# Optimization experiments

Measured on AMD Instinct MI355X. Metric: run time of the kernel, lower is better.

Reference implementation:

```python
import jax, jax.numpy as jnp
import numpy as np

DIM = 2048
N_HEADS = 16
N_KV_HEADS = 4
HEAD_DIM = DIM // N_HEADS  # 128
N_REP = N_HEADS // N_KV_HEADS
LENS = [1024, 2048, 512, 512]
T = sum(LENS)  # 4096 packed tokens
THETA = 10000.0
NEG_INF = -1e30


def setup_inputs() -> dict:
    key = jax.random.key(0)
    ks = jax.random.split(key, 5)
    sd = 1.0 / np.sqrt(DIM)
    x = jax.random.normal(ks[0], (T, DIM), dtype=jnp.float32)
    wq = jax.random.normal(ks[1], (DIM, N_HEADS * HEAD_DIM), dtype=jnp.float32) * sd
    wk = jax.random.normal(ks[2], (DIM, N_KV_HEADS * HEAD_DIM), dtype=jnp.float32) * sd
    wv = jax.random.normal(ks[3], (DIM, N_KV_HEADS * HEAD_DIM), dtype=jnp.float32) * sd
    wo = jax.random.normal(ks[4], (N_HEADS * HEAD_DIM, DIM), dtype=jnp.float32) * sd
    # varlen packing metadata: per-token segment id and in-sequence position
    seq_ids = jnp.asarray(np.repeat(np.arange(len(LENS)), LENS), dtype=jnp.int32)
    pos = jnp.asarray(np.concatenate([np.arange(l) for l in LENS]), dtype=jnp.float32)
    # rotary frequencies (precompute_freqs_cis), gathered per packed token
    inv_freq = 1.0 / (THETA ** (np.arange(0, HEAD_DIM, 2, dtype=np.float32) / HEAD_DIM))  # [HEAD_DIM//2]
    angles = pos[:, None] * jnp.asarray(inv_freq)[None, :]  # [T, HEAD_DIM//2]
    freqs_cos = jnp.cos(angles)
    freqs_sin = jnp.sin(angles)
    return {"x": x, "wq": wq, "wk": wk, "wv": wv, "wo": wo,
            "freqs_cos": freqs_cos, "freqs_sin": freqs_sin, "seq_ids": seq_ids}


def _apply_rope(t, cos, sin):
    # t: [T, H, D]; rotate interleaved (even, odd) pairs, matching torch view_as_complex
    tr = t.reshape(t.shape[0], t.shape[1], HEAD_DIM // 2, 2)
    x0, x1 = tr[..., 0], tr[..., 1]
    c = cos[:, None, :]
    s = sin[:, None, :]
    o0 = x0 * c - x1 * s
    o1 = x0 * s + x1 * c
    return jnp.stack([o0, o1], axis=-1).reshape(t.shape)


def reference(x, wq, wk, wv, wo, freqs_cos, freqs_sin, seq_ids):
    Tn = x.shape[0]
    xq = (x @ wq).reshape(Tn, N_HEADS, HEAD_DIM)
    xk = (x @ wk).reshape(Tn, N_KV_HEADS, HEAD_DIM)
    xv = (x @ wv).reshape(Tn, N_KV_HEADS, HEAD_DIM)
    xq = _apply_rope(xq, freqs_cos, freqs_sin)
    xk = _apply_rope(xk, freqs_cos, freqs_sin)
    # GQA: repeat kv heads
    xk = jnp.repeat(xk, N_REP, axis=1)  # [T, N_HEADS, D]
    xv = jnp.repeat(xv, N_REP, axis=1)
    scale = 1.0 / jnp.sqrt(jnp.float32(HEAD_DIM))
    scores = jnp.einsum('thd,shd->hts', xq, xk) * scale  # [H, T, T]
    idx = jnp.arange(Tn)
    # varlen causal mask: same sequence AND key index <= query index
    allowed = (seq_ids[:, None] == seq_ids[None, :]) & (idx[None, :] <= idx[:, None])
    scores = jnp.where(allowed[None, :, :], scores, NEG_INF)
    attn = jax.nn.softmax(scores, axis=-1)
    out = jnp.einsum('hts,shd->thd', attn, xv).reshape(Tn, N_HEADS * HEAD_DIM)
    return out @ wo
```

## Files before the change

### kernel.cpp

```cpp
#include <hip/hip_runtime.h>
#include <hip/hip_bf16.h>


typedef __attribute__((ext_vector_type(4))) float f32x4;
typedef __attribute__((ext_vector_type(8))) short short8;
typedef __attribute__((ext_vector_type(4))) short short4v;

#define DEV __device__ __forceinline__

DEV short f2bf(float f) {
  __hip_bfloat16 h = __float2bfloat16(f);
  union { __hip_bfloat16 h; short s; } u; u.h = h; return u.s;
}
DEV float bf2f(short s) {
  union { short s; __hip_bfloat16 h; } u; u.s = s; return __bfloat162float(u.h);
}

DEV void gload_lds16(const void* g, void* l) {
  __builtin_amdgcn_global_load_lds(
      (const __attribute__((address_space(1))) void*)g,
      (__attribute__((address_space(3))) void*)l, 16, 0, 0);
}

__global__ void cast_x(const float* __restrict__ in, short* __restrict__ out, int n4) {
  int i = blockIdx.x * 256 + threadIdx.x;
  if (i >= n4) return;
  f32x4 v = ((const f32x4*)in)[i];
  short4v o;
  o[0] = f2bf(v[0]); o[1] = f2bf(v[1]); o[2] = f2bf(v[2]); o[3] = f2bf(v[3]);
  ((short4v*)out)[i] = o;
}

__global__ void transpose_cast_f32(const float* __restrict__ in, short* __restrict__ out,
                                   int R, int C) {
  __shared__ float tile[32][33];
  int bc = blockIdx.x * 32, br = blockIdx.y * 32;
  int tx = threadIdx.x, ty = threadIdx.y;
#pragma unroll
  for (int i = 0; i < 32; i += 8)
    tile[ty + i][tx] = in[(size_t)(br + ty + i) * C + bc + tx];
  __syncthreads();
#pragma unroll
  for (int i = 0; i < 32; i += 8)
    out[(size_t)(bc + ty + i) * R + br + tx] = f2bf(tile[tx][ty + i]);
}

__global__ void transpose_bf16(const short* __restrict__ in, short* __restrict__ out,
                               int R, int C, int ldi, int ldo) {
  __shared__ short tile[32][33];
  int bc = blockIdx.x * 32, br = blockIdx.y * 32;
  int tx = threadIdx.x, ty = threadIdx.y;
#pragma unroll
  for (int i = 0; i < 32; i += 8)
    tile[ty + i][tx] = in[(size_t)(br + ty + i) * ldi + bc + tx];
  __syncthreads();
#pragma unroll
  for (int i = 0; i < 32; i += 8)
    out[(size_t)(bc + ty + i) * ldo + br + tx] = tile[tx][ty + i];
}

__global__ void rope_kernel(short* __restrict__ qkv,
                            const float* __restrict__ fc, const float* __restrict__ fs) {
  int t = blockIdx.x;
  int g = threadIdx.x;
  int gi, col;
  if (g < 256) { int h = g >> 4; gi = g & 15; col = h * 128 + gi * 8; }
  else { int kh = (g - 256) >> 4; gi = (g - 256) & 15; col = 2048 + kh * 128 + gi * 8; }
  size_t base = (size_t)t * 3072 + col;
  short8 v = *(short8*)(qkv + base);
  f32x4 c = *(const f32x4*)(fc + (size_t)t * 64 + gi * 4);
  f32x4 s = *(const f32x4*)(fs + (size_t)t * 64 + gi * 4);
#pragma unroll
  for (int e = 0; e < 4; ++e) {
    float x0 = bf2f(v[2 * e]), x1 = bf2f(v[2 * e + 1]);
    float o0 = x0 * c[e] - x1 * s[e];
    float o1 = x0 * s[e] + x1 * c[e];
    v[2 * e] = f2bf(o0); v[2 * e + 1] = f2bf(o1);
  }
  *(short8*)(qkv + base) = v;
}

template <typename OutT>
__global__ __launch_bounds__(256, 2) void gemm_bt(const short* __restrict__ A,
                                                  const short* __restrict__ BT,
                                                  OutT* __restrict__ C,
                                                  int M, int N, int K,
                                                  int lda, int ldb, int ldc) {
  __shared__ short As[2][128 * 32];
  __shared__ short Bs[2][128 * 32];
  const int tid = threadIdx.x;
  const int wave = tid >> 6, lane = tid & 63;
  const int wr = wave >> 1, wc = wave & 1;
  const int bm = blockIdx.y, bn = blockIdx.x;
  const int l15 = lane & 15, l4 = lane >> 4;
  f32x4 acc[4][4] = {};

  auto stage = [&](int buf, int kt) {
#pragma unroll
    for (int i = 0; i < 2; ++i) {
      int j = wave * 2 + i;
      int row = j * 16 + (lane >> 2);
      int lg = (lane & 3) ^ ((row >> 1) & 3);
      gload_lds16(A + (size_t)(bm * 128 + row) * lda + kt + lg * 8, &As[buf][j * 512]);
      gload_lds16(BT + (size_t)(bn * 128 + row) * ldb + kt + lg * 8, &Bs[buf][j * 512]);
    }
  };

  stage(0, 0);
  __syncthreads();

  const int nk = K >> 5;
  for (int t = 0; t < nk; ++t) {
    const int cur = t & 1;
    if (t + 1 < nk) stage(cur ^ 1, (t + 1) * 32);

    short8 a[4], b[4];
#pragma unroll
    for (int m = 0; m < 4; ++m) {
      int row = wr * 64 + m * 16 + l15;
      int ph = l4 ^ ((row >> 1) & 3);
      a[m] = *(const short8*)(&As[cur][row * 32 + ph * 8]);
    }
#pragma unroll
    for (int n = 0; n < 4; ++n) {
      int row = wc * 64 + n * 16 + l15;
      int ph = l4 ^ ((row >> 1) & 3);
      b[n] = *(const short8*)(&Bs[cur][row * 32 + ph * 8]);
    }
    __builtin_amdgcn_s_setprio(1);
#pragma unroll
    for (int m = 0; m < 4; ++m)
#pragma unroll
      for (int n = 0; n < 4; ++n)
        acc[m][n] = __builtin_amdgcn_mfma_f32_16x16x32_bf16(a[m], b[n], acc[m][n], 0, 0, 0);
    __builtin_amdgcn_s_setprio(0);
    __syncthreads();
  }

#pragma unroll
  for (int m = 0; m < 4; ++m) {
    int row0 = bm * 128 + wr * 64 + m * 16 + l4 * 4;
#pragma unroll
    for (int n = 0; n < 4; ++n) {
      int col = bn * 128 + wc * 64 + n * 16 + l15;
#pragma unroll
      for (int r = 0; r < 4; ++r) {
        float v = acc[m][n][r];
        if constexpr (sizeof(OutT) == 4) C[(size_t)(row0 + r) * ldc + col] = v;
        else                             C[(size_t)(row0 + r) * ldc + col] = f2bf(v);
      }
    }
  }
}

__constant__ int QPERM[64] = {
    47, 46, 45, 44, 43, 42, 41, 40, 39, 38, 37, 36, 35, 34, 33, 32,
    31, 15, 30, 14, 29, 13, 28, 12, 27, 11, 26, 10, 25,  9, 24,  8,
    23,  7, 55, 63, 22,  6, 54, 62, 21,  5, 53, 61, 20,  4, 52, 60,
    19,  3, 51, 59, 18,  2, 50, 58, 17,  1, 49, 57, 16,  0, 48, 56};

__global__ __launch_bounds__(256, 3) void attn_kernel(const short* __restrict__ qkv,
                                                      const short* __restrict__ vt,
                                                      short* __restrict__ out) {
  __shared__ short Ks[64 * 128];
  __shared__ short Vs[128 * 64];
  __shared__ short Ps[4][16 * 64];
  const int tid = threadIdx.x;
  const int wave = tid >> 6, lane = tid & 63;
  const int l15 = lane & 15, l4 = lane >> 4;
  const int h = blockIdx.x;
  const int qi = QPERM[blockIdx.y];
  const int q0 = qi * 64;
  const int kvh = h >> 2;

  const int trow = q0 + wave * 16 + l15;
  short8 qf[4];
#pragma unroll
  for (int kk = 0; kk < 4; ++kk)
    qf[kk] = *(const short8*)(qkv + (size_t)trow * 3072 + h * 128 + kk * 32 + l4 * 8);

  f32x4 of[8] = {};
  float mrun[4], lrun[4];
#pragma unroll
  for (int r = 0; r < 4; ++r) { mrun[r] = -1e30f; lrun[r] = 0.f; }

  const int kstart = (q0 >= 3584) ? 3584 : (q0 >= 3072) ? 3072 : (q0 >= 1024) ? 1024 : 0;
  const int nt = ((q0 + 64) - kstart) >> 6;
  short* Pw = Ps[wave];

  const int krow0 = wave * 4 + (lane >> 4);
  const int ksl   = (lane & 15) ^ (krow0 & 7);
  const int vrow0 = wave * 8 + (lane >> 3);
  const int vsl   = (lane & 7) ^ (vrow0 & 7);

  short8 kreg[4], vreg[4];
  auto load_regs = [&](int kt) {
#pragma unroll
    for (int j = 0; j < 4; ++j) {
      kreg[j] = *(const short8*)(qkv + (size_t)(kt + j * 16 + krow0) * 3072 + 2048 +
                                 kvh * 128 + ksl * 8);
      vreg[j] = *(const short8*)(vt + (size_t)(kvh * 128 + j * 32 + vrow0) * 4096 + kt +
                                 vsl * 8);
    }
  };
  auto write_lds = [&]() {
#pragma unroll
    for (int j = 0; j < 4; ++j) {
      *(short8*)(Ks + (j * 16 + krow0) * 128 + (lane & 15) * 8) = kreg[j];
      *(short8*)(Vs + (j * 32 + vrow0) * 64 + (lane & 7) * 8) = vreg[j];
    }
  };

  load_regs(kstart);
  write_lds();
  __syncthreads();

  constexpr float SCL2 = 0.08838834764831845f * 1.4426950408889634f;

  for (int ti = 0; ti < nt; ++ti) {
    const int kt = kstart + ti * 64;
    if (ti + 1 < nt) load_regs(kt + 64);

    f32x4 sfr[4] = {};
    __builtin_amdgcn_s_setprio(1);
#pragma unroll
    for (int st = 0; st < 4; ++st) {
      int srow = st * 16 + l15;
#pragma unroll
      for (int kk = 0; kk < 4; ++kk) {
        int ph = (kk * 4 + l4) ^ (srow & 7);
        short8 kfrag = *(const short8*)(Ks + srow * 128 + ph * 8);
        sfr[st] = __builtin_amdgcn_mfma_f32_16x16x32_bf16(qf[kk], kfrag, sfr[st], 0, 0, 0);
      }
    }
    __builtin_amdgcn_s_setprio(0);

    float p[4][4], mx[4];
#pragma unroll
    for (int r = 0; r < 4; ++r) {
      int tg = q0 + wave * 16 + l4 * 4 + r;
      float m = -1e30f;
#pragma unroll
      for (int st = 0; st < 4; ++st) {
        float v = sfr[st][r] * SCL2;
        if (kt + st * 16 + l15 > tg) v = -1e30f;
        p[st][r] = v;
        m = fmaxf(m, v);
      }
#pragma unroll
      for (int off = 1; off < 16; off <<= 1) m = fmaxf(m, __shfl_xor(m, off));
      mx[r] = m;
    }
    bool need = (mx[0] > mrun[0] + 8.f) || (mx[1] > mrun[1] + 8.f) ||
                (mx[2] > mrun[2] + 8.f) || (mx[3] > mrun[3] + 8.f);
    if (__any(need)) {
#pragma unroll
      for (int r = 0; r < 4; ++r) {
        float mn = fmaxf(mrun[r], mx[r]);
        float scl = __builtin_amdgcn_exp2f(mrun[r] - mn);
        lrun[r] *= scl;
        mrun[r] = mn;
#pragma unroll
        for (int nd = 0; nd < 8; ++nd) of[nd][r] *= scl;
      }
    }
#pragma unroll
    for (int r = 0; r < 4; ++r) {
      float sum = 0.f;
#pragma unroll
      for (int st = 0; st < 4; ++st) {
        p[st][r] = __builtin_amdgcn_exp2f(p[st][r] - mrun[r]);
        sum += p[st][r];
      }
#pragma unroll
      for (int off = 1; off < 16; off <<= 1) sum += __shfl_xor(sum, off);
      lrun[r] += sum;
    }

#pragma unroll
    for (int st = 0; st < 4; ++st)
#pragma unroll
      for (int r = 0; r < 4; ++r) {
        int row = l4 * 4 + r;
        int col = st * 16 + l15;
        int ph = (col >> 3) ^ (row & 7);
        Pw[row * 64 + ph * 8 + (col & 7)] = f2bf(p[st][r]);
      }

    __builtin_amdgcn_s_setprio(1);
#pragma unroll
    for (int kc = 0; kc < 2; ++kc) {
      int pph = (kc * 4 + l4) ^ (l15 & 7);
      short8 pa = *(const short8*)(Pw + l15 * 64 + pph * 8);
#pragma unroll
      for (int nd = 0; nd < 8; ++nd) {
        int vrow = nd * 16 + l15;
        int vph = (kc * 4 + l4) ^ (vrow & 7);
        short8 vf = *(const short8*)(Vs + vrow * 64 + vph * 8);
        of[nd] = __builtin_amdgcn_mfma_f32_16x16x32_bf16(pa, vf, of[nd], 0, 0, 0);
      }
    }
    __builtin_amdgcn_s_setprio(0);

    __syncthreads();
    if (ti + 1 < nt) write_lds();
    __syncthreads();
  }

#pragma unroll
  for (int r = 0; r < 4; ++r) {
    float inv = 1.0f / lrun[r];
    int tg = q0 + wave * 16 + l4 * 4 + r;
#pragma unroll
    for (int nd = 0; nd < 8; ++nd)
      out[(size_t)tg * 2048 + h * 128 + nd * 16 + l15] = f2bf(of[nd][r] * inv);
  }
}

extern "C" void kernel_launch(void* const* d_in, const int* in_sizes, int n_in,
                              void* d_out, int out_size, void* d_ws, size_t ws_size,
                              hipStream_t stream) {
  (void)in_sizes; (void)n_in; (void)out_size; (void)ws_size;
  const float* x  = (const float*)d_in[0];
  const float* wq = (const float*)d_in[1];
  const float* wk = (const float*)d_in[2];
  const float* wv = (const float*)d_in[3];
  const float* wo = (const float*)d_in[4];
  const float* fc = (const float*)d_in[5];
  const float* fs = (const float*)d_in[6];

  char* p = (char*)d_ws;
  short* xb  = (short*)p; p += (size_t)4096 * 2048 * 2;
  short* wT  = (short*)p; p += (size_t)3072 * 2048 * 2;
  short* woT = (short*)p; p += (size_t)2048 * 2048 * 2;
  short* qkv = (short*)p; p += (size_t)4096 * 3072 * 2;
  short* vt  = (short*)p; p += (size_t)512 * 4096 * 2;
  short* ao  = (short*)p; p += (size_t)4096 * 2048 * 2;
  float* outp = (float*)d_out;

  dim3 tb(32, 8);
  cast_x<<<8192, 256, 0, stream>>>(x, xb, 2097152);
  transpose_cast_f32<<<dim3(64, 64), tb, 0, stream>>>(wq, wT,               2048, 2048);
  transpose_cast_f32<<<dim3(16, 64), tb, 0, stream>>>(wk, wT + 2048 * 2048, 2048, 512);
  transpose_cast_f32<<<dim3(16, 64), tb, 0, stream>>>(wv, wT + 2560 * 2048, 2048, 512);
  transpose_cast_f32<<<dim3(64, 64), tb, 0, stream>>>(wo, woT,              2048, 2048);
  gemm_bt<short><<<dim3(24, 32), 256, 0, stream>>>(xb, wT, qkv, 4096, 3072, 2048,
                                                   2048, 2048, 3072);
  rope_kernel<<<4096, 320, 0, stream>>>(qkv, fc, fs);
  transpose_bf16<<<dim3(16, 128), tb, 0, stream>>>(qkv + 2560, vt, 4096, 512, 3072, 4096);
  attn_kernel<<<dim3(16, 64), 256, 0, stream>>>(qkv, vt, ao);
  gemm_bt<float><<<dim3(16, 32), 256, 0, stream>>>(ao, woT, outp, 4096, 2048, 2048,
                                                   2048, 2048, 2048);
}
```

Before: 342.7 us.

## Read K/V fragments directly from global memory and swizzle GEMM block order

The attention kernel drops its shared-memory staging of K and V tiles. Each wave now loads its MFMA fragments straight from global memory (relying on L1/L2 reuse across the four waves), which removes the LDS writes and both block barriers per tile. The GEMM gets an XCD-style block-index swizzle for better L2 locality and its launch bound rises to 3 blocks per CU. The cost is that all four waves now issue redundant global loads for K/V, with no software prefetch, so latency may be exposed.

```diff
diff --git a/kernel.cpp b/kernel.cpp
--- a/kernel.cpp
+++ b/kernel.cpp
@@ -81,7 +81,7 @@
 }
 
 template <typename OutT>
-__global__ __launch_bounds__(256, 2) void gemm_bt(const short* __restrict__ A,
+__global__ __launch_bounds__(256, 3) void gemm_bt(const short* __restrict__ A,
                                                   const short* __restrict__ BT,
                                                   OutT* __restrict__ C,
                                                   int M, int N, int K,
@@ -91,7 +91,10 @@
   const int tid = threadIdx.x;
   const int wave = tid >> 6, lane = tid & 63;
   const int wr = wave >> 1, wc = wave & 1;
-  const int bm = blockIdx.y, bn = blockIdx.x;
+  const int nwg = gridDim.x * gridDim.y;
+  const int bid = blockIdx.y * gridDim.x + blockIdx.x;
+  const int swz = (bid & 7) * (nwg >> 3) + (bid >> 3);
+  const int bm = swz / gridDim.x, bn = swz % gridDim.x;
   const int l15 = lane & 15, l4 = lane >> 4;
   f32x4 acc[4][4] = {};
 
@@ -162,8 +165,6 @@
 __global__ __launch_bounds__(256, 3) void attn_kernel(const short* __restrict__ qkv,
                                                       const short* __restrict__ vt,
                                                       short* __restrict__ out) {
-  __shared__ short Ks[64 * 128];
-  __shared__ short Vs[128 * 64];
   __shared__ short Ps[4][16 * 64];
   const int tid = threadIdx.x;
   const int wave = tid >> 6, lane = tid & 63;
@@ -188,48 +189,22 @@
   const int nt = ((q0 + 64) - kstart) >> 6;
   short* Pw = Ps[wave];
 
-  const int krow0 = wave * 4 + (lane >> 4);
-  const int ksl   = (lane & 15) ^ (krow0 & 7);
-  const int vrow0 = wave * 8 + (lane >> 3);
-  const int vsl   = (lane & 7) ^ (vrow0 & 7);
-
-  short8 kreg[4], vreg[4];
-  auto load_regs = [&](int kt) {
-#pragma unroll
-    for (int j = 0; j < 4; ++j) {
-      kreg[j] = *(const short8*)(qkv + (size_t)(kt + j * 16 + krow0) * 3072 + 2048 +
-                                 kvh * 128 + ksl * 8);
-      vreg[j] = *(const short8*)(vt + (size_t)(kvh * 128 + j * 32 + vrow0) * 4096 + kt +
-                                 vsl * 8);
-    }
-  };
-  auto write_lds = [&]() {
-#pragma unroll
-    for (int j = 0; j < 4; ++j) {
-      *(short8*)(Ks + (j * 16 + krow0) * 128 + (lane & 15) * 8) = kreg[j];
-      *(short8*)(Vs + (j * 32 + vrow0) * 64 + (lane & 7) * 8) = vreg[j];
-    }
-  };
-
-  load_regs(kstart);
-  write_lds();
-  __syncthreads();
+  const short* Kbase = qkv + 2048 + kvh * 128 + (size_t)l15 * 3072 + l4 * 8;
+  const short* Vbase = vt + (size_t)(kvh * 128 + l15) * 4096 + l4 * 8;
 
   constexpr float SCL2 = 0.08838834764831845f * 1.4426950408889634f;
 
   for (int ti = 0; ti < nt; ++ti) {
     const int kt = kstart + ti * 64;
-    if (ti + 1 < nt) load_regs(kt + 64);
 
     f32x4 sfr[4] = {};
     __builtin_amdgcn_s_setprio(1);
 #pragma unroll
     for (int st = 0; st < 4; ++st) {
-      int srow = st * 16 + l15;
+      const short* krow = Kbase + (size_t)(kt + st * 16) * 3072;
 #pragma unroll
       for (int kk = 0; kk < 4; ++kk) {
-        int ph = (kk * 4 + l4) ^ (srow & 7);
-        short8 kfrag = *(const short8*)(Ks + srow * 128 + ph * 8);
+        short8 kfrag = *(const short8*)(krow + kk * 32);
         sfr[st] = __builtin_amdgcn_mfma_f32_16x16x32_bf16(qf[kk], kfrag, sfr[st], 0, 0, 0);
       }
     }
@@ -292,19 +267,14 @@
     for (int kc = 0; kc < 2; ++kc) {
       int pph = (kc * 4 + l4) ^ (l15 & 7);
       short8 pa = *(const short8*)(Pw + l15 * 64 + pph * 8);
+      const short* vcol = Vbase + kt + kc * 32;
 #pragma unroll
       for (int nd = 0; nd < 8; ++nd) {
-        int vrow = nd * 16 + l15;
-        int vph = (kc * 4 + l4) ^ (vrow & 7);
-        short8 vf = *(const short8*)(Vs + vrow * 64 + vph * 8);
+        short8 vf = *(const short8*)(vcol + (size_t)(nd * 16) * 4096);
         of[nd] = __builtin_amdgcn_mfma_f32_16x16x32_bf16(pa, vf, of[nd], 0, 0, 0);
       }
     }
     __builtin_amdgcn_s_setprio(0);
-
-    __syncthreads();
-    if (ti + 1 < nt) write_lds();
-    __syncthreads();
   }
 
 #pragma unroll
```

Result: slower. 510.5 us (+49.0%).
